# Performance work log

Measured on AMD Instinct MI355X. Metric: run time of the kernel, lower is better.

## Reference

```python
import jax, jax.numpy as jnp
import numpy as np

B, NQ, NK, QS, KS, H, VD = 16, 64, 512, 256, 256, 256, 256


def setup_inputs() -> dict:
    key = jax.random.key(0)
    k1, k2, k3, k4, k5, k6, k7 = jax.random.split(key, 7)
    return {
        "queries": jax.random.normal(k1, (B, NQ, QS), dtype=jnp.float32),
        "keys": jax.random.normal(k2, (B, NK, KS), dtype=jnp.float32),
        "values": jax.random.normal(k3, (B, NK, VD), dtype=jnp.float32),
        "valid_lens": jax.random.randint(k4, (B,), 1, NK + 1, dtype=jnp.int32),
        # learned params (nn.Linear with bias=False): W_q [QS,H], W_k [KS,H], w_v [H]
        "W_q": jax.random.normal(k5, (QS, H), dtype=jnp.float32) / np.sqrt(QS),
        "W_k": jax.random.normal(k6, (KS, H), dtype=jnp.float32) / np.sqrt(KS),
        "w_v": jax.random.normal(k7, (H,), dtype=jnp.float32) / np.sqrt(H),
    }


def reference(queries, keys, values, valid_lens, W_q, W_k, w_v):
    # project: q [B,nq,H], k [B,nk,H]
    q = jnp.einsum("bqd,dh->bqh", queries, W_q)
    k = jnp.einsum("bkd,dh->bkh", keys, W_k)
    # broadcast-add -> tanh -> score reduction via w_v: [B,nq,nk]
    features = jnp.tanh(q[:, :, None, :] + k[:, None, :, :])  # [B,nq,nk,H]
    scores = jnp.einsum("bqkh,h->bqk", features, w_v)
    # masked softmax over keys (positions >= valid_len masked out)
    mask = jnp.arange(scores.shape[-1])[None, None, :] < valid_lens[:, None, None]
    scores = jnp.where(mask, scores, -1e6)
    attn = jax.nn.softmax(scores, axis=-1)
    # weighted sum of values (dropout p=0 / eval mode => identity)
    return jnp.einsum("bqk,bkv->bqv", attn, values)
```

## Files before the change

### kernel.cpp

```cpp
#include <hip/hip_runtime.h>
#include <hip/hip_bf16.h>

#define BB 16
#define NQ 64
#define NK 512
#define HD 256

typedef __attribute__((ext_vector_type(8))) short short8;
typedef __attribute__((ext_vector_type(4))) float f32x4;

__device__ __forceinline__ ushort bf16_rne(float v) {
    unsigned u = __float_as_uint(v);
    return (ushort)((u + 0x7FFFu + ((u >> 16) & 1u)) >> 16);
}
__device__ __forceinline__ float bf16_to_f(ushort h) {
    return __uint_as_float(((unsigned)h) << 16);
}

__global__ __launch_bounds__(256) void wconv(
    const float* __restrict__ wq, const float* __restrict__ wk,
    ushort* __restrict__ wqh, ushort* __restrict__ wql,
    ushort* __restrict__ wkh, ushort* __restrict__ wkl)
{
    int widx = blockIdx.x * 256 + threadIdx.x;
    const float* W; ushort *wh, *wl;
    if (widx < 16384) { W = wq; wh = wqh; wl = wql; }
    else { W = wk; wh = wkh; wl = wkl; widx -= 16384; }
    int n  = widx >> 6;
    int k4 = (widx & 63) * 4;
    ushort hh[4], ll[4];
    #pragma unroll
    for (int c = 0; c < 4; ++c) {
        float v = W[(k4 + c) * 256 + n];
        hh[c] = bf16_rne(v);
        ll[c] = bf16_rne(v - bf16_to_f(hh[c]));
    }
    *(ushort4*)&wh[n * 256 + k4] = make_ushort4(hh[0], hh[1], hh[2], hh[3]);
    *(ushort4*)&wl[n * 256 + k4] = make_ushort4(ll[0], ll[1], ll[2], ll[3]);
}

__global__ __launch_bounds__(256, 2) void proj_fused(
    const float* __restrict__ queries, const float* __restrict__ keys,
    const ushort* __restrict__ wqh, const ushort* __restrict__ wql,
    const ushort* __restrict__ wkh, const ushort* __restrict__ wkl,
    float* __restrict__ qp, float* __restrict__ kp, float scale)
{
    __shared__ ushort AsH[64 * 64], AsL[64 * 64];
    __shared__ ushort BsH[64 * 64], BsL[64 * 64];

    const float* A; const ushort *Bh, *Bl; float* C; int rows0;
    const int bx = blockIdx.x;
    if (bx < 16) { A = queries; Bh = wqh; Bl = wql; C = qp; rows0 = bx * 64; }
    else         { A = keys;    Bh = wkh; Bl = wkl; C = kp; rows0 = (bx - 16) * 64; }
    const int cols0 = blockIdx.y * 64;

    const int t = threadIdx.x, lane = t & 63, wave = t >> 6;
    const int quad = lane >> 4, l15 = lane & 15;
    const int sr  = t >> 2;
    const int sc2 = (t & 3) * 2;

    f32x4 acc[4];
    #pragma unroll
    for (int j = 0; j < 4; ++j) acc[j] = (f32x4){0.f, 0.f, 0.f, 0.f};

    for (int k0 = 0; k0 < 256; k0 += 64) {
        const float* arow = &A[(size_t)(rows0 + sr) * 256 + k0 + sc2 * 8];
        float4 a0 = *(const float4*)&arow[0];
        float4 a1 = *(const float4*)&arow[4];
        float4 a2 = *(const float4*)&arow[8];
        float4 a3 = *(const float4*)&arow[12];
        const ushort* bhp = &Bh[(size_t)(cols0 + sr) * 256 + k0 + sc2 * 8];
        const ushort* blp = &Bl[(size_t)(cols0 + sr) * 256 + k0 + sc2 * 8];
        short8 b0h = *(const short8*)&bhp[0];
        short8 b1h = *(const short8*)&bhp[8];
        short8 b0l = *(const short8*)&blp[0];
        short8 b1l = *(const short8*)&blp[8];

        __syncthreads();

        float av[16] = {a0.x, a0.y, a0.z, a0.w, a1.x, a1.y, a1.z, a1.w,
                        a2.x, a2.y, a2.z, a2.w, a3.x, a3.y, a3.z, a3.w};
        short8 ah0, ah1, al0, al1;
        #pragma unroll
        for (int e = 0; e < 8; ++e) {
            ushort h0 = bf16_rne(av[e]);
            ushort h1 = bf16_rne(av[8 + e]);
            ah0[e] = (short)h0;
            ah1[e] = (short)h1;
            al0[e] = (short)bf16_rne(av[e] - bf16_to_f(h0));
            al1[e] = (short)bf16_rne(av[8 + e] - bf16_to_f(h1));
        }
        {
            int s0 = sr * 8 + ((sc2 + 0) ^ (sr & 7));
            int s1 = sr * 8 + ((sc2 + 1) ^ (sr & 7));
            *(short8*)&AsH[s0 * 8] = ah0;
            *(short8*)&AsH[s1 * 8] = ah1;
            *(short8*)&AsL[s0 * 8] = al0;
            *(short8*)&AsL[s1 * 8] = al1;
            *(short8*)&BsH[s0 * 8] = b0h;
            *(short8*)&BsH[s1 * 8] = b1h;
            *(short8*)&BsL[s0 * 8] = b0l;
            *(short8*)&BsL[s1 * 8] = b1l;
        }
        __syncthreads();

        #pragma unroll
        for (int ks = 0; ks < 2; ++ks) {
            const int c = ks * 4 + quad;
            short8 aH, aL, bH[4], bL[4];
            {
                int r = wave * 16 + l15;
                int slot = r * 8 + (c ^ (r & 7));
                aH = *(const short8*)&AsH[slot * 8];
                aL = *(const short8*)&AsL[slot * 8];
            }
            #pragma unroll
            for (int ns = 0; ns < 4; ++ns) {
                int n = ns * 16 + l15;
                int slot = n * 8 + (c ^ (n & 7));
                bH[ns] = *(const short8*)&BsH[slot * 8];
                bL[ns] = *(const short8*)&BsL[slot * 8];
            }
            #pragma unroll
            for (int ns = 0; ns < 4; ++ns)
                acc[ns] = __builtin_amdgcn_mfma_f32_16x16x32_bf16(aH, bH[ns], acc[ns], 0, 0, 0);
            #pragma unroll
            for (int ns = 0; ns < 4; ++ns)
                acc[ns] = __builtin_amdgcn_mfma_f32_16x16x32_bf16(aL, bH[ns], acc[ns], 0, 0, 0);
            #pragma unroll
            for (int ns = 0; ns < 4; ++ns)
                acc[ns] = __builtin_amdgcn_mfma_f32_16x16x32_bf16(aH, bL[ns], acc[ns], 0, 0, 0);
        }
    }

    const int rbase = rows0 + wave * 16 + quad * 4;
    #pragma unroll
    for (int ns = 0; ns < 4; ++ns) {
        int col = cols0 + ns * 16 + l15;
        #pragma unroll
        for (int r = 0; r < 4; ++r)
            C[(size_t)(rbase + r) * 256 + col] =
                __builtin_amdgcn_exp2f(acc[ns][r] * scale);
    }
}

__global__ __launch_bounds__(256) void score_pv_seg2(
    const float* __restrict__ qp,
    const float* __restrict__ kp,
    const float* __restrict__ values,
    const int*   __restrict__ vlens,
    const float* __restrict__ w_v,
    float* __restrict__ pO,
    float* __restrict__ pM,
    float* __restrict__ pL)
{
    __shared__ float eq[8][260];
    __shared__ float wv[HD];
    __shared__ float Ps[8][66];
    __shared__ float part[4][8][260];

    const int b   = blockIdx.x & 15;
    const int qt  = blockIdx.x >> 4;
    const int seg = blockIdx.y;
    const int vl  = vlens[b];
    if (seg * 64 >= vl) return;

    const int t = threadIdx.x, lane = t & 63, wave = t >> 6;

    const float* qsrc = qp + ((size_t)b * NQ + qt * 8) * HD;
    #pragma unroll
    for (int i = 0; i < 2; ++i) {
        int idx = i * 256 + t;
        int row = idx >> 6, c4 = (idx & 63) * 4;
        *(float4*)&eq[row][c4] = *(const float4*)&qsrc[(size_t)row * HD + c4];
    }
    if (t < 64) *(float4*)&wv[t * 4] = *(const float4*)&w_v[t * 4];
    __syncthreads();

    float Wsum;
    {
        float ws = wv[lane] + wv[lane + 64] + wv[lane + 128] + wv[lane + 192];
        #pragma unroll
        for (int off = 32; off; off >>= 1) ws += __shfl_xor(ws, off);
        Wsum = ws;
    }

    const int key = wave * 16 + (lane >> 2);
    const int ch  = lane & 3;
    const int kg  = seg * 64 + key;
    const float* krow = kp + ((size_t)b * NK + kg) * HD + ch * 4;

    float s[8] = {0.f, 0.f, 0.f, 0.f, 0.f, 0.f, 0.f, 0.f};
    #pragma unroll
    for (int j = 0; j < 16; ++j) {
        const int h = j * 16 + ch * 4;
        float4 ek = *(const float4*)&krow[j * 16];
        float4 w4 = *(const float4*)&wv[h];
        #pragma unroll
        for (int qi = 0; qi < 8; ++qi) {
            float4 q4 = *(const float4*)&eq[qi][h];
            float p0 = fmaf(q4.x, ek.x, 1.f);
            float p1 = fmaf(q4.y, ek.y, 1.f);
            float p2 = fmaf(q4.z, ek.z, 1.f);
            float p3 = fmaf(q4.w, ek.w, 1.f);
            float d01 = p0 * p1;
            float d23 = p2 * p3;
            float n01 = fmaf(w4.x, p1, w4.y * p0);
            float n23 = fmaf(w4.z, p3, w4.w * p2);
            float num = fmaf(d01, n23, d23 * n01);
            float r   = __builtin_amdgcn_rcpf(d01 * d23);
            s[qi] = fmaf(num, r, s[qi]);
        }
    }
    #pragma unroll
    for (int qi = 0; qi < 8; ++qi) {
        s[qi] += __shfl_xor(s[qi], 1);
        s[qi] += __shfl_xor(s[qi], 2);
    }
    if (ch == 0) {
        const bool masked = (kg >= vl);
        #pragma unroll
        for (int qi = 0; qi < 8; ++qi)
            Ps[qi][key] = masked ? -1e6f : fmaf(-2.f, s[qi], Wsum);
    }
    __syncthreads();

    const float L2E = 1.4426950408889634f;
    #pragma unroll
    for (int r = 0; r < 2; ++r) {
        const int row = wave * 2 + r;
        float sv = Ps[row][lane];
        float m = sv;
        #pragma unroll
        for (int off = 32; off; off >>= 1) m = fmaxf(m, __shfl_xor(m, off));
        float e = __builtin_amdgcn_exp2f((sv - m) * L2E);
        float l = e;
        #pragma unroll
        for (int off = 32; off; off >>= 1) l += __shfl_xor(l, off);
        Ps[row][lane] = e;
        if (lane == 0) {
            size_t mi = (((size_t)(b * 8 + qt) * 8 + seg)) * 8 + row;
            pM[mi] = m;
            pL[mi] = l;
        }
    }
    __syncthreads();

    f32x4 acc[8];
    #pragma unroll
    for (int qi = 0; qi < 8; ++qi) acc[qi] = (f32x4){0.f, 0.f, 0.f, 0.f};
    const float* vbase = values + ((size_t)b * NK + seg * 64 + wave * 16) * HD;
    #pragma unroll
    for (int i = 0; i < 16; ++i) {
        float4 v = *(const float4*)&vbase[(size_t)i * HD + lane * 4];
        #pragma unroll
        for (int qi = 0; qi < 8; ++qi) {
            float p = Ps[qi][wave * 16 + i];
            acc[qi][0] = fmaf(p, v.x, acc[qi][0]);
            acc[qi][1] = fmaf(p, v.y, acc[qi][1]);
            acc[qi][2] = fmaf(p, v.z, acc[qi][2]);
            acc[qi][3] = fmaf(p, v.w, acc[qi][3]);
        }
    }
    #pragma unroll
    for (int qi = 0; qi < 8; ++qi)
        *(f32x4*)&part[wave][qi][lane * 4] = acc[qi];
    __syncthreads();

    const size_t ob = (((size_t)(b * 8 + qt) * 8 + seg)) * 8 * 256;
    #pragma unroll
    for (int i = 0; i < 2; ++i) {
        int idx = i * 256 + t;
        int qi = idx >> 6, c4 = (idx & 63) * 4;
        float4 p0 = *(const float4*)&part[0][qi][c4];
        float4 p1 = *(const float4*)&part[1][qi][c4];
        float4 p2 = *(const float4*)&part[2][qi][c4];
        float4 p3 = *(const float4*)&part[3][qi][c4];
        float4 o;
        o.x = (p0.x + p1.x) + (p2.x + p3.x);
        o.y = (p0.y + p1.y) + (p2.y + p3.y);
        o.z = (p0.z + p1.z) + (p2.z + p3.z);
        o.w = (p0.w + p1.w) + (p2.w + p3.w);
        *(float4*)&pO[ob + (size_t)qi * 256 + c4] = o;
    }
}

__global__ __launch_bounds__(256) void combine_seg2(
    const float* __restrict__ pO, const float* __restrict__ pM,
    const float* __restrict__ pL, const int* __restrict__ vlens,
    float* __restrict__ out)
{
    const int b  = blockIdx.x >> 6;
    const int q  = blockIdx.x & 63;
    const int t  = threadIdx.x;
    const int vl = vlens[b];
    const int nc = (vl + 63) >> 6;
    const int qt = q >> 3, qi = q & 7;
    const float L2E = 1.4426950408889634f;

    const size_t base = (size_t)(b * 8 + qt) * 8;

    float mi[8], li[8];
    float m = -3e38f;
    #pragma unroll
    for (int i = 0; i < 8; ++i) {
        if (i < nc) {
            mi[i] = pM[(base + i) * 8 + qi];
            li[i] = pL[(base + i) * 8 + qi];
            m = fmaxf(m, mi[i]);
        }
    }
    float L = 0.f, wi[8];
    #pragma unroll
    for (int i = 0; i < 8; ++i) {
        if (i < nc) {
            wi[i] = __builtin_amdgcn_exp2f((mi[i] - m) * L2E);
            L = fmaf(li[i], wi[i], L);
        }
    }
    float acc = 0.f;
    #pragma unroll
    for (int i = 0; i < 8; ++i) {
        if (i < nc) acc = fmaf(wi[i], pO[((base + i) * 8 + qi) * 256 + t], acc);
    }
    out[((size_t)(b * 64 + q)) * 256 + t] = acc * __builtin_amdgcn_rcpf(L);
}

extern "C" void kernel_launch(void* const* d_in, const int* in_sizes, int n_in,
                              void* d_out, int out_size, void* d_ws, size_t ws_size,
                              hipStream_t stream) {
    const float* queries = (const float*)d_in[0];
    const float* keys    = (const float*)d_in[1];
    const float* values  = (const float*)d_in[2];
    const int*   vlens   = (const int*)d_in[3];
    const float* W_q     = (const float*)d_in[4];
    const float* W_k     = (const float*)d_in[5];
    const float* w_v     = (const float*)d_in[6];
    float* out = (float*)d_out;

    float*  kp  = (float*)d_ws;
    float*  qp  = kp + (size_t)BB * NK * HD;
    float*  pO  = qp + (size_t)BB * NQ * HD;
    float*  pM  = pO + (size_t)BB * 8 * 8 * 8 * 256;
    float*  pL  = pM + (size_t)BB * 8 * 8 * 8;
    ushort* wqh = (ushort*)(pL + (size_t)BB * 8 * 8 * 8);
    ushort* wql = wqh + 65536;
    ushort* wkh = wql + 65536;
    ushort* wkl = wkh + 65536;

    const float SC = 2.885390081777927f;

    wconv<<<dim3(128), 256, 0, stream>>>(W_q, W_k, wqh, wql, wkh, wkl);
    proj_fused<<<dim3(144, 4), 256, 0, stream>>>(queries, keys,
                                                 wqh, wql, wkh, wkl,
                                                 qp, kp, SC);
    score_pv_seg2<<<dim3(128, 8), 256, 0, stream>>>(qp, kp, values, vlens, w_v,
                                                    pO, pM, pL);
    combine_seg2<<<dim3(BB * NQ), 256, 0, stream>>>(pO, pM, pL, vlens, out);
}
```

Measured before the change: 114.8 us.

## Split score kernel hidden dimension across two wave groups with 512-thread blocks

```diff
diff --git a/kernel.cpp b/kernel.cpp
--- a/kernel.cpp
+++ b/kernel.cpp
@@ -144,7 +144,7 @@
     }
 }
 
-__global__ __launch_bounds__(256) void score_pv_seg2(
+__global__ __launch_bounds__(512, 4) void score_pv_seg3(
     const float* __restrict__ qp,
     const float* __restrict__ kp,
     const float* __restrict__ values,
@@ -157,6 +157,7 @@
     __shared__ float eq[8][260];
     __shared__ float wv[HD];
     __shared__ float Ps[8][66];
+    __shared__ float sP[8][66];
     __shared__ float part[4][8][260];
 
     const int b   = blockIdx.x & 15;
@@ -166,12 +167,20 @@
     if (seg * 64 >= vl) return;
 
     const int t = threadIdx.x, lane = t & 63, wave = t >> 6;
+    const int kq = wave & 3;
+    const int hh = wave >> 2;
+    const int key = kq * 16 + (lane >> 2);
+    const int ch  = lane & 3;
+    const int kg  = seg * 64 + key;
+
+    const float* krow = kp + ((size_t)b * NK + kg) * HD + hh * 128 + ch * 4;
+    float4 ek[8];
+    #pragma unroll
+    for (int j = 0; j < 8; ++j) ek[j] = *(const float4*)&krow[j * 16];
 
     const float* qsrc = qp + ((size_t)b * NQ + qt * 8) * HD;
-    #pragma unroll
-    for (int i = 0; i < 2; ++i) {
-        int idx = i * 256 + t;
-        int row = idx >> 6, c4 = (idx & 63) * 4;
+    {
+        int row = t >> 6, c4 = (t & 63) * 4;
         *(float4*)&eq[row][c4] = *(const float4*)&qsrc[(size_t)row * HD + c4];
     }
     if (t < 64) *(float4*)&wv[t * 4] = *(const float4*)&w_v[t * 4];
@@ -185,24 +194,19 @@
         Wsum = ws;
     }
 
-    const int key = wave * 16 + (lane >> 2);
-    const int ch  = lane & 3;
-    const int kg  = seg * 64 + key;
-    const float* krow = kp + ((size_t)b * NK + kg) * HD + ch * 4;
-
     float s[8] = {0.f, 0.f, 0.f, 0.f, 0.f, 0.f, 0.f, 0.f};
     #pragma unroll
-    for (int j = 0; j < 16; ++j) {
-        const int h = j * 16 + ch * 4;
-        float4 ek = *(const float4*)&krow[j * 16];
+    for (int j = 0; j < 8; ++j) {
+        const int h = hh * 128 + j * 16 + ch * 4;
+        float4 e4 = ek[j];
         float4 w4 = *(const float4*)&wv[h];
         #pragma unroll
         for (int qi = 0; qi < 8; ++qi) {
             float4 q4 = *(const float4*)&eq[qi][h];
-            float p0 = fmaf(q4.x, ek.x, 1.f);
-            float p1 = fmaf(q4.y, ek.y, 1.f);
-            float p2 = fmaf(q4.z, ek.z, 1.f);
-            float p3 = fmaf(q4.w, ek.w, 1.f);
+            float p0 = fmaf(q4.x, e4.x, 1.f);
+            float p1 = fmaf(q4.y, e4.y, 1.f);
+            float p2 = fmaf(q4.z, e4.z, 1.f);
+            float p3 = fmaf(q4.w, e4.w, 1.f);
             float d01 = p0 * p1;
             float d23 = p2 * p3;
             float n01 = fmaf(w4.x, p1, w4.y * p0);
@@ -217,18 +221,23 @@
         s[qi] += __shfl_xor(s[qi], 1);
         s[qi] += __shfl_xor(s[qi], 2);
     }
-    if (ch == 0) {
+    if (hh == 1 && ch == 0) {
+        #pragma unroll
+        for (int qi = 0; qi < 8; ++qi) sP[qi][key] = s[qi];
+    }
+    __syncthreads();
+    if (hh == 0 && ch == 0) {
         const bool masked = (kg >= vl);
         #pragma unroll
         for (int qi = 0; qi < 8; ++qi)
-            Ps[qi][key] = masked ? -1e6f : fmaf(-2.f, s[qi], Wsum);
+            Ps[qi][key] = masked ? -1e6f
+                                 : fmaf(-2.f, s[qi] + sP[qi][key], Wsum);
     }
     __syncthreads();
 
     const float L2E = 1.4426950408889634f;
-    #pragma unroll
-    for (int r = 0; r < 2; ++r) {
-        const int row = wave * 2 + r;
+    {
+        const int row = wave;
         float sv = Ps[row][lane];
         float m = sv;
         #pragma unroll
@@ -246,32 +255,30 @@
     }
     __syncthreads();
 
-    f32x4 acc[8];
-    #pragma unroll
-    for (int qi = 0; qi < 8; ++qi) acc[qi] = (f32x4){0.f, 0.f, 0.f, 0.f};
-    const float* vbase = values + ((size_t)b * NK + seg * 64 + wave * 16) * HD;
+    f32x4 acc[4];
+    #pragma unroll
+    for (int r = 0; r < 4; ++r) acc[r] = (f32x4){0.f, 0.f, 0.f, 0.f};
+    const float* vbase = values + ((size_t)b * NK + seg * 64 + kq * 16) * HD;
     #pragma unroll
     for (int i = 0; i < 16; ++i) {
         float4 v = *(const float4*)&vbase[(size_t)i * HD + lane * 4];
         #pragma unroll
-        for (int qi = 0; qi < 8; ++qi) {
-            float p = Ps[qi][wave * 16 + i];
-            acc[qi][0] = fmaf(p, v.x, acc[qi][0]);
-            acc[qi][1] = fmaf(p, v.y, acc[qi][1]);
-            acc[qi][2] = fmaf(p, v.z, acc[qi][2]);
-            acc[qi][3] = fmaf(p, v.w, acc[qi][3]);
-        }
-    }
-    #pragma unroll
-    for (int qi = 0; qi < 8; ++qi)
-        *(f32x4*)&part[wave][qi][lane * 4] = acc[qi];
+        for (int r = 0; r < 4; ++r) {
+            float p = Ps[hh * 4 + r][kq * 16 + i];
+            acc[r][0] = fmaf(p, v.x, acc[r][0]);
+            acc[r][1] = fmaf(p, v.y, acc[r][1]);
+            acc[r][2] = fmaf(p, v.z, acc[r][2]);
+            acc[r][3] = fmaf(p, v.w, acc[r][3]);
+        }
+    }
+    #pragma unroll
+    for (int r = 0; r < 4; ++r)
+        *(f32x4*)&part[kq][hh * 4 + r][lane * 4] = acc[r];
     __syncthreads();
 
     const size_t ob = (((size_t)(b * 8 + qt) * 8 + seg)) * 8 * 256;
-    #pragma unroll
-    for (int i = 0; i < 2; ++i) {
-        int idx = i * 256 + t;
-        int qi = idx >> 6, c4 = (idx & 63) * 4;
+    {
+        int qi = t >> 6, c4 = (t & 63) * 4;
         float4 p0 = *(const float4*)&part[0][qi][c4];
         float4 p1 = *(const float4*)&part[1][qi][c4];
         float4 p2 = *(const float4*)&part[2][qi][c4];
@@ -354,7 +361,7 @@
     proj_fused<<<dim3(144, 4), 256, 0, stream>>>(queries, keys,
                                                  wqh, wql, wkh, wkl,
                                                  qp, kp, SC);
-    score_pv_seg2<<<dim3(128, 8), 256, 0, stream>>>(qp, kp, values, vlens, w_v,
+    score_pv_seg3<<<dim3(128, 8), 512, 0, stream>>>(qp, kp, values, vlens, w_v,
                                                     pO, pM, pL);
     combine_seg2<<<dim3(BB * NQ), 256, 0, stream>>>(pO, pM, pL, vlens, out);
 }
```

Measured after the change: 111.5 us. 1.03x faster.

## Drop max-subtraction softmax and prefetch key/value rows into registers

Applied to the files above, without the earlier changes.

```diff
diff --git a/kernel.cpp b/kernel.cpp
--- a/kernel.cpp
+++ b/kernel.cpp
@@ -144,14 +144,13 @@
     }
 }
 
-__global__ __launch_bounds__(256) void score_pv_seg2(
+__global__ __launch_bounds__(256, 3) void score_pv_seg4(
     const float* __restrict__ qp,
     const float* __restrict__ kp,
     const float* __restrict__ values,
     const int*   __restrict__ vlens,
     const float* __restrict__ w_v,
     float* __restrict__ pO,
-    float* __restrict__ pM,
     float* __restrict__ pL)
 {
     __shared__ float eq[8][260];
@@ -166,6 +165,14 @@
     if (seg * 64 >= vl) return;
 
     const int t = threadIdx.x, lane = t & 63, wave = t >> 6;
+    const int key = wave * 16 + (lane >> 2);
+    const int ch  = lane & 3;
+    const int kg  = seg * 64 + key;
+
+    const float* krow = kp + ((size_t)b * NK + kg) * HD + ch * 4;
+    float4 ek[16];
+    #pragma unroll
+    for (int j = 0; j < 16; ++j) ek[j] = *(const float4*)&krow[j * 16];
 
     const float* qsrc = qp + ((size_t)b * NQ + qt * 8) * HD;
     #pragma unroll
@@ -185,24 +192,19 @@
         Wsum = ws;
     }
 
-    const int key = wave * 16 + (lane >> 2);
-    const int ch  = lane & 3;
-    const int kg  = seg * 64 + key;
-    const float* krow = kp + ((size_t)b * NK + kg) * HD + ch * 4;
-
     float s[8] = {0.f, 0.f, 0.f, 0.f, 0.f, 0.f, 0.f, 0.f};
     #pragma unroll
     for (int j = 0; j < 16; ++j) {
         const int h = j * 16 + ch * 4;
-        float4 ek = *(const float4*)&krow[j * 16];
+        float4 e4 = ek[j];
         float4 w4 = *(const float4*)&wv[h];
         #pragma unroll
         for (int qi = 0; qi < 8; ++qi) {
             float4 q4 = *(const float4*)&eq[qi][h];
-            float p0 = fmaf(q4.x, ek.x, 1.f);
-            float p1 = fmaf(q4.y, ek.y, 1.f);
-            float p2 = fmaf(q4.z, ek.z, 1.f);
-            float p3 = fmaf(q4.w, ek.w, 1.f);
+            float p0 = fmaf(q4.x, e4.x, 1.f);
+            float p1 = fmaf(q4.y, e4.y, 1.f);
+            float p2 = fmaf(q4.z, e4.z, 1.f);
+            float p3 = fmaf(q4.w, e4.w, 1.f);
             float d01 = p0 * p1;
             float d23 = p2 * p3;
             float n01 = fmaf(w4.x, p1, w4.y * p0);
@@ -212,6 +214,14 @@
             s[qi] = fmaf(num, r, s[qi]);
         }
     }
+
+    const float* vbase = values + ((size_t)b * NK + seg * 64 + wave * 16) * HD;
+    float4 vv[16];
+    #pragma unroll
+    for (int i = 0; i < 16; ++i)
+        vv[i] = *(const float4*)&vbase[(size_t)i * HD + lane * 4];
+
+    const float L2E = 1.4426950408889634f;
     #pragma unroll
     for (int qi = 0; qi < 8; ++qi) {
         s[qi] += __shfl_xor(s[qi], 1);
@@ -220,39 +230,20 @@
     if (ch == 0) {
         const bool masked = (kg >= vl);
         #pragma unroll
-        for (int qi = 0; qi < 8; ++qi)
-            Ps[qi][key] = masked ? -1e6f : fmaf(-2.f, s[qi], Wsum);
+        for (int qi = 0; qi < 8; ++qi) {
+            float sv = fmaf(-2.f, s[qi], Wsum);
+            Ps[qi][key] = masked ? 0.f
+                                 : __builtin_amdgcn_exp2f(sv * L2E);
+        }
     }
     __syncthreads();
 
-    const float L2E = 1.4426950408889634f;
-    #pragma unroll
-    for (int r = 0; r < 2; ++r) {
-        const int row = wave * 2 + r;
-        float sv = Ps[row][lane];
-        float m = sv;
-        #pragma unroll
-        for (int off = 32; off; off >>= 1) m = fmaxf(m, __shfl_xor(m, off));
-        float e = __builtin_amdgcn_exp2f((sv - m) * L2E);
-        float l = e;
-        #pragma unroll
-        for (int off = 32; off; off >>= 1) l += __shfl_xor(l, off);
-        Ps[row][lane] = e;
-        if (lane == 0) {
-            size_t mi = (((size_t)(b * 8 + qt) * 8 + seg)) * 8 + row;
-            pM[mi] = m;
-            pL[mi] = l;
-        }
-    }
-    __syncthreads();
-
     f32x4 acc[8];
     #pragma unroll
     for (int qi = 0; qi < 8; ++qi) acc[qi] = (f32x4){0.f, 0.f, 0.f, 0.f};
-    const float* vbase = values + ((size_t)b * NK + seg * 64 + wave * 16) * HD;
     #pragma unroll
     for (int i = 0; i < 16; ++i) {
-        float4 v = *(const float4*)&vbase[(size_t)i * HD + lane * 4];
+        float4 v = vv[i];
         #pragma unroll
         for (int qi = 0; qi < 8; ++qi) {
             float p = Ps[qi][wave * 16 + i];
@@ -262,6 +253,17 @@
             acc[qi][3] = fmaf(p, v.w, acc[qi][3]);
         }
     }
+
+    #pragma unroll
+    for (int r = 0; r < 2; ++r) {
+        const int row = wave * 2 + r;
+        float l = Ps[row][lane];
+        #pragma unroll
+        for (int off = 32; off; off >>= 1) l += __shfl_xor(l, off);
+        if (lane == 0)
+            pL[(((size_t)(b * 8 + qt) * 8 + seg)) * 8 + row] = l;
+    }
+
     #pragma unroll
     for (int qi = 0; qi < 8; ++qi)
         *(f32x4*)&part[wave][qi][lane * 4] = acc[qi];
@@ -285,43 +287,25 @@
     }
 }
 
-__global__ __launch_bounds__(256) void combine_seg2(
-    const float* __restrict__ pO, const float* __restrict__ pM,
-    const float* __restrict__ pL, const int* __restrict__ vlens,
-    float* __restrict__ out)
+__global__ __launch_bounds__(256) void combine_seg3(
+    const float* __restrict__ pO, const float* __restrict__ pL,
+    const int* __restrict__ vlens, float* __restrict__ out)
 {
     const int b  = blockIdx.x >> 6;
     const int q  = blockIdx.x & 63;
     const int t  = threadIdx.x;
-    const int vl = vlens[b];
-    const int nc = (vl + 63) >> 6;
+    const int nc = (vlens[b] + 63) >> 6;
     const int qt = q >> 3, qi = q & 7;
-    const float L2E = 1.4426950408889634f;
 
     const size_t base = (size_t)(b * 8 + qt) * 8;
 
-    float mi[8], li[8];
-    float m = -3e38f;
+    float L = 0.f, acc = 0.f;
     #pragma unroll
     for (int i = 0; i < 8; ++i) {
         if (i < nc) {
-            mi[i] = pM[(base + i) * 8 + qi];
-            li[i] = pL[(base + i) * 8 + qi];
-            m = fmaxf(m, mi[i]);
-        }
-    }
-    float L = 0.f, wi[8];
-    #pragma unroll
-    for (int i = 0; i < 8; ++i) {
-        if (i < nc) {
-            wi[i] = __builtin_amdgcn_exp2f((mi[i] - m) * L2E);
-            L = fmaf(li[i], wi[i], L);
-        }
-    }
-    float acc = 0.f;
-    #pragma unroll
-    for (int i = 0; i < 8; ++i) {
-        if (i < nc) acc = fmaf(wi[i], pO[((base + i) * 8 + qi) * 256 + t], acc);
+            L   += pL[(base + i) * 8 + qi];
+            acc += pO[((base + i) * 8 + qi) * 256 + t];
+        }
     }
     out[((size_t)(b * 64 + q)) * 256 + t] = acc * __builtin_amdgcn_rcpf(L);
 }
@@ -341,8 +325,7 @@
     float*  kp  = (float*)d_ws;
     float*  qp  = kp + (size_t)BB * NK * HD;
     float*  pO  = qp + (size_t)BB * NQ * HD;
-    float*  pM  = pO + (size_t)BB * 8 * 8 * 8 * 256;
-    float*  pL  = pM + (size_t)BB * 8 * 8 * 8;
+    float*  pL  = pO + (size_t)BB * 8 * 8 * 8 * 256;
     ushort* wqh = (ushort*)(pL + (size_t)BB * 8 * 8 * 8);
     ushort* wql = wqh + 65536;
     ushort* wkh = wql + 65536;
@@ -354,7 +337,7 @@
     proj_fused<<<dim3(144, 4), 256, 0, stream>>>(queries, keys,
                                                  wqh, wql, wkh, wkl,
                                                  qp, kp, SC);
-    score_pv_seg2<<<dim3(128, 8), 256, 0, stream>>>(qp, kp, values, vlens, w_v,
-                                                    pO, pM, pL);
-    combine_seg2<<<dim3(BB * NQ), 256, 0, stream>>>(pO, pM, pL, vlens, out);
-}
+    score_pv_seg4<<<dim3(128, 8), 256, 0, stream>>>(qp, kp, values, vlens, w_v,
+                                                    pO, pL);
+    combine_seg3<<<dim3(BB * NQ), 256, 0, stream>>>(pO, pL, vlens, out);
+}
```

Result: slower. 120.7 us (+5.2%).
